# Optimization experiments

Hardware: AMD Instinct MI355X
Metric: run time of the kernel (lower is better)

## Reference

```python
import jax, jax.numpy as jnp
import numpy as np

INPUT_DIM = 128
HIDDEN_DIM = 64
BATCH = 256
SEQ_LEN = 1024


def _projectors(n):
    n_half = n // 2
    S = jnp.zeros((n, n), jnp.float32)
    S = S.at[:n_half, n_half:].set(jnp.eye(n_half))
    S = S.at[n_half:, :n_half].set(jnp.eye(n_half))
    I = jnp.eye(n, dtype=jnp.float32)
    return (I + S) / 2.0, (I - S) / 2.0


def setup_inputs() -> dict:
    key = jax.random.key(0)
    ks = jax.random.split(key, 7)
    x = jax.random.normal(ks[0], (BATCH, SEQ_LEN, INPUT_DIM), jnp.float32)
    A_plus = jax.random.normal(ks[1], (HIDDEN_DIM, HIDDEN_DIM), jnp.float32) * 0.1
    A_minus = jax.random.normal(ks[2], (HIDDEN_DIM, HIDDEN_DIM), jnp.float32) * 0.1
    # nn.Linear default init: U(-1/sqrt(fan_in), 1/sqrt(fan_in))
    b_in = 1.0 / np.sqrt(INPUT_DIM)
    W_in_w = jax.random.uniform(ks[3], (HIDDEN_DIM, INPUT_DIM), jnp.float32, -b_in, b_in)
    W_in_b = jax.random.uniform(ks[4], (HIDDEN_DIM,), jnp.float32, -b_in, b_in)
    b_out = 1.0 / np.sqrt(HIDDEN_DIM)
    W_out_w = jax.random.uniform(ks[5], (INPUT_DIM, HIDDEN_DIM), jnp.float32, -b_out, b_out)
    W_out_b = jax.random.uniform(ks[6], (INPUT_DIM,), jnp.float32, -b_out, b_out)
    bias = jnp.zeros((HIDDEN_DIM,), jnp.float32)
    return {"x": x, "A_plus": A_plus, "A_minus": A_minus,
            "W_in_w": W_in_w, "W_in_b": W_in_b,
            "W_out_w": W_out_w, "W_out_b": W_out_b, "bias": bias}


def reference(x, A_plus, A_minus, W_in_w, W_in_b, W_out_w, W_out_b, bias):
    B, T, _ = x.shape
    H = bias.shape[0]
    P_plus, P_minus = _projectors(H)
    # W_comm = P+ A+ P+ + P- A- P-
    W_comm = P_plus @ A_plus @ P_plus + P_minus @ A_minus @ P_minus
    # Precompute input projection for all timesteps (one big GEMM): (B,T,H)
    inp = jnp.einsum('bti,hi->bth', x, W_in_w) + W_in_b + bias
    inp_t = jnp.transpose(inp, (1, 0, 2))  # (T,B,H)

    def step(h, u_t):
        h = jnp.tanh(h @ W_comm.T + u_t)
        return h, None

    h0 = jnp.zeros((B, H), x.dtype)
    hidden, _ = jax.lax.scan(step, h0, inp_t)
    predictions = hidden @ W_out_w.T + W_out_b  # (B, input_dim)
    return predictions, hidden
```

## Files before the change

kernel.cpp:

```cpp
#include <hip/hip_runtime.h>
#include <hip/hip_bf16.h>

#define BB 256
#define TT 1024
#define II 128
#define HH 64

#define PRESCALE 2.8853900817779268f

typedef float    f32x4_t __attribute__((ext_vector_type(4)));
typedef _Float16 h16x2   __attribute__((ext_vector_type(2)));
typedef _Float16 h16x4   __attribute__((ext_vector_type(4)));
typedef _Float16 h16x8   __attribute__((ext_vector_type(8)));
typedef __fp16   p16x2   __attribute__((ext_vector_type(2)));

union UH2 { unsigned u; h16x2 h; p16x2 p; };
union U4H8 { uint4 u; h16x8 h; };
union B128 { uint4 u; h16x2 h[4]; };

__device__ __forceinline__ float tanh_pre(float a){
  float e = __builtin_amdgcn_exp2f(a);
  return __builtin_fmaf(-2.0f, __builtin_amdgcn_rcpf(1.0f + e), 1.0f);
}

#if __has_builtin(__builtin_amdgcn_fdot2)
__device__ __forceinline__ float fdot2f(h16x2 a, h16x2 b, float c){
  return __builtin_amdgcn_fdot2(a, b, c, false);
}
#else
__device__ __forceinline__ float fdot2f(h16x2 a, h16x2 b, float c){
  return __builtin_fmaf((float)a[1], (float)b[1], __builtin_fmaf((float)a[0], (float)b[0], c));
}
#endif

__global__ void k_prep(const float* __restrict__ Ap, const float* __restrict__ Am,
                       const float* __restrict__ Winw,
                       const float* __restrict__ Winb, const float* __restrict__ bias,
                       float* __restrict__ wsf, unsigned* __restrict__ whf,
                       unsigned short* __restrict__ wsb){
  const int tid = threadIdx.x;
  for (int e = tid; e < 4096; e += 256){
    int i = e >> 6, j = e & 63;
    int is = i ^ 32, js = j ^ 32;
    float wp = Ap[i*64+j] + Ap[i*64+js] + Ap[is*64+j] + Ap[is*64+js];
    float wm = Am[i*64+j] - Am[i*64+js] - Am[is*64+j] + Am[is*64+js];
    wsf[e] = 0.25f * (wp + wm) * PRESCALE;
  }
  if (tid < 64) wsf[4096 + tid] = (Winb[tid] + bias[tid]) * PRESCALE;
  for (int e = tid; e < 8192; e += 256){
    int j = e & 7, lane = (e >> 3) & 63, fidx = e >> 9;
    int ks = fidx >> 2, nt = fidx & 3, l15 = lane & 15, q = lane >> 4;
    union { _Float16 f; unsigned short s; } cv;
    cv.f = (_Float16)(Winw[(nt*16 + l15)*II + ks*32 + q*8 + j] * PRESCALE);
    wsb[e] = cv.s;
  }
  __syncthreads();
  for (int e = tid; e < 2048; e += 256){
    int i = e >> 5, jp = e & 31;
    UH2 p;
    p.h[0] = (_Float16)wsf[i*64 + 2*jp];
    p.h[1] = (_Float16)wsf[i*64 + 2*jp + 1];
    whf[e] = p.u;
  }
}

__global__ __launch_bounds__(256, 1) void k_fused(const float* __restrict__ x,
                                                  const float* __restrict__ wsf,
                                                  const unsigned* __restrict__ whf,
                                                  const unsigned short* __restrict__ wsb,
                                                  const float* __restrict__ Wout,
                                                  const float* __restrict__ Woutb,
                                                  float* __restrict__ out){
  extern __shared__ unsigned char smem[];
  unsigned short* Us    = (unsigned short*)smem;
  unsigned*       flags = (unsigned*)(smem + 131072);
  unsigned*       Hb    = (unsigned*)(smem + 131072 + 256);

  const int b    = blockIdx.x;
  const int tid  = threadIdx.x;
  const int lane = tid & 63;
  const int wave = tid >> 6;
  const int l15  = lane & 15;
  const int q    = lane >> 4;

  if (tid < 64) flags[tid] = 0u;
  __syncthreads();

  if (wave != 0){
    h16x8 bfr[4][4];
    #pragma unroll
    for (int ks = 0; ks < 4; ++ks)
      #pragma unroll
      for (int nt = 0; nt < 4; ++nt)
        bfr[ks][nt] = *(const h16x8*)(wsb + ((ks*4 + nt)*64 + lane)*8);

    float bcv[4];
    #pragma unroll
    for (int nt = 0; nt < 4; ++nt) bcv[nt] = wsf[4096 + nt*16 + l15];

    const float* xb = x + (long)b * (TT * II);

    #pragma unroll 1
    for (int tile = wave - 1; tile < 64; tile += 3){
      const int trow = tile * 16;
      const float* xa = xb + (trow + l15) * II + q*8;
      h16x8 afr[4];
      #pragma unroll
      for (int ks = 0; ks < 4; ++ks){
        float4 a0 = *(const float4*)(xa + ks*32);
        float4 a1 = *(const float4*)(xa + ks*32 + 4);
        U4H8 v;
        UH2 p0, p1, p2, p3;
        p0.p = __builtin_amdgcn_cvt_pkrtz(a0.x, a0.y);
        p1.p = __builtin_amdgcn_cvt_pkrtz(a0.z, a0.w);
        p2.p = __builtin_amdgcn_cvt_pkrtz(a1.x, a1.y);
        p3.p = __builtin_amdgcn_cvt_pkrtz(a1.z, a1.w);
        v.u.x = p0.u; v.u.y = p1.u; v.u.z = p2.u; v.u.w = p3.u;
        afr[ks] = v.h;
      }
      f32x4_t acc[4];
      #pragma unroll
      for (int nt = 0; nt < 4; ++nt){
        acc[nt][0]=bcv[nt]; acc[nt][1]=bcv[nt]; acc[nt][2]=bcv[nt]; acc[nt][3]=bcv[nt];
      }
      #pragma unroll
      for (int ks = 0; ks < 4; ++ks){
        #pragma unroll
        for (int nt = 0; nt < 4; ++nt){
          acc[nt] = __builtin_amdgcn_mfma_f32_16x16x32_f16(afr[ks], bfr[ks][nt], acc[nt], 0, 0, 0);
        }
      }
      const int tg = tile*4 + q;
      #pragma unroll
      for (int nt = 0; nt < 4; ++nt){
        UH2 lo, hi;
        lo.p = __builtin_amdgcn_cvt_pkrtz(acc[nt][0], acc[nt][1]);
        hi.p = __builtin_amdgcn_cvt_pkrtz(acc[nt][2], acc[nt][3]);
        uint2 pk; pk.x = lo.u; pk.y = hi.u;
        *(uint2*)&Us[(tg*64 + nt*16 + l15) * 4] = pk;
      }
      __threadfence_block();
      if (lane == 0)
        __hip_atomic_store(&flags[tile], 1u, __ATOMIC_RELEASE, __HIP_MEMORY_SCOPE_WORKGROUP);
    }
    return;
  }

  h16x2 w[32];
  {
    const uint4* wr = (const uint4*)(whf + lane * 32);
    #pragma unroll
    for (int j4 = 0; j4 < 8; ++j4){
      uint4 v = wr[j4];
      UH2 c0, c1, c2, c3;
      c0.u = v.x; c1.u = v.y; c2.u = v.z; c3.u = v.w;
      w[4*j4+0] = c0.h; w[4*j4+1] = c1.h; w[4*j4+2] = c2.h; w[4*j4+3] = c3.h;
    }
  }

  while (!__hip_atomic_load(&flags[0], __ATOMIC_ACQUIRE, __HIP_MEMORY_SCOPE_WORKGROUP)) {}

  const h16x4* Ul = (const h16x4*)Us;
  h16x4 uc = Ul[0*64 + lane];
  h16x4 u1 = Ul[1*64 + lane];

  const bool wlane = !(lane & 1);

  float h = 0.0f;
  int last_ready = 0;
  #pragma unroll 1
  for (int tile = 0; tile < 64; ++tile){
    int wt = tile + 1; if (wt > 63) wt = 63;
    if (wt > last_ready){
      while (!__hip_atomic_load(&flags[wt], __ATOMIC_ACQUIRE, __HIP_MEMORY_SCOPE_WORKGROUP)) {}
      last_ready = wt;
    }
    #pragma unroll
    for (int tgl = 0; tgl < 4; ++tgl){
      const int tg = tile*4 + tgl;
      int tp = tg + 2; if (tp > TT/4 - 1) tp = TT/4 - 1;
      h16x4 u2 = Ul[tp*64 + lane];
      float ug0 = (float)uc[0], ug1 = (float)uc[1], ug2 = (float)uc[2], ug3 = (float)uc[3];
      #pragma unroll
      for (int g = 0; g < 4; ++g){
        float ugv = (g==0) ? ug0 : (g==1) ? ug1 : (g==2) ? ug2 : ug3;
        unsigned nbu = (unsigned)__builtin_amdgcn_mov_dpp(__float_as_uint(h), 0xB1, 0xF, 0xF, true);
        UH2 hp; hp.p = __builtin_amdgcn_cvt_pkrtz(h, __uint_as_float(nbu));
        if (wlane) Hb[lane >> 1] = hp.u;
        __asm__ volatile("" ::: "memory");
        __builtin_amdgcn_sched_barrier(0);
        B128 hv[8];
        const uint4* Hr = (const uint4*)Hb;
        #pragma unroll
        for (int r = 0; r < 8; ++r) hv[r].u = Hr[r];
        float a0 = ugv, a1 = 0.0f, a2 = 0.0f, a3 = 0.0f;
        #pragma unroll
        for (int jp = 0; jp < 32; jp += 4){
          a0 = fdot2f(w[jp+0], hv[(jp+0)>>2].h[(jp+0)&3], a0);
          a1 = fdot2f(w[jp+1], hv[(jp+1)>>2].h[(jp+1)&3], a1);
          a2 = fdot2f(w[jp+2], hv[(jp+2)>>2].h[(jp+2)&3], a2);
          a3 = fdot2f(w[jp+3], hv[(jp+3)>>2].h[(jp+3)&3], a3);
        }
        h = tanh_pre((a0 + a1) + (a2 + a3));
      }
      uc = u1; u1 = u2;
    }
  }

  unsigned hu = __float_as_uint(h);
  float p0 = Woutb[lane];
  float p1 = Woutb[lane + 64];
  #pragma unroll 8
  for (int j = 0; j < 64; ++j){
    float hj = __uint_as_float(__builtin_amdgcn_readlane(hu, j));
    p0 = __builtin_fmaf(Wout[lane * HH + j],        hj, p0);
    p1 = __builtin_fmaf(Wout[(lane + 64) * HH + j], hj, p1);
  }
  out[b * 128 + lane]           = p0;
  out[b * 128 + 64 + lane]      = p1;
  out[BB * 128 + b * 64 + lane] = h;
}

extern "C" void kernel_launch(void* const* d_in, const int* in_sizes, int n_in,
                              void* d_out, int out_size, void* d_ws, size_t ws_size,
                              hipStream_t stream){
  const float* x     = (const float*)d_in[0];
  const float* Ap    = (const float*)d_in[1];
  const float* Am    = (const float*)d_in[2];
  const float* Winw  = (const float*)d_in[3];
  const float* Winb  = (const float*)d_in[4];
  const float* Woutw = (const float*)d_in[5];
  const float* Woutb = (const float*)d_in[6];
  const float* bias  = (const float*)d_in[7];

  float*          wsf = (float*)d_ws;
  unsigned*       whf = (unsigned*)((char*)d_ws + 16640);
  unsigned short* wsb = (unsigned short*)((char*)d_ws + 24832);

  float* out = (float*)d_out;

  hipFuncSetAttribute((const void*)k_fused,
                      hipFuncAttributeMaxDynamicSharedMemorySize, 131456);

  hipLaunchKernelGGL(k_prep,  dim3(1),   dim3(256), 0,      stream, Ap, Am, Winw, Winb, bias, wsf, whf, wsb);
  hipLaunchKernelGGL(k_fused, dim3(BB),  dim3(256), 131456, stream, x, wsf, whf, wsb, Woutw, Woutb, out);
}
```

Before: 339.5 us.

## Block-diagonalize recurrent matrix via symmetric/antisymmetric projector basis

Uses the projector structure of W_comm to split the 64x64 recurrence into two independent 32x32 blocks acting on the sum and difference of hidden halves. Each lane forms h±h_swap with a permlane32 swap, writes the packed values to a per-half LDS slot, and does 16 fdot2 instead of 32. A second swap recombines the outputs into the original basis. This halves the per-step dot-product work and LDS reads on the serial critical path, at the cost of two cross-half swaps per step and extra fp16 rounding of the combined values.

Measured after the change: 311.4 us. 8.3% less time.

```diff
diff --git a/kernel.cpp b/kernel.cpp
--- a/kernel.cpp
+++ b/kernel.cpp
@@ -30,6 +30,18 @@
 #else
 __device__ __forceinline__ float fdot2f(h16x2 a, h16x2 b, float c){
   return __builtin_fmaf((float)a[1], (float)b[1], __builtin_fmaf((float)a[0], (float)b[0], c));
+}
+#endif
+
+#if __has_builtin(__builtin_amdgcn_permlane32_swap)
+__device__ __forceinline__ float half_swap(float v){
+  unsigned vu = __float_as_uint(v);
+  auto r = __builtin_amdgcn_permlane32_swap(vu, vu, false, false);
+  return __uint_as_float(((unsigned)r[0]) ^ ((unsigned)r[1]) ^ vu);
+}
+#else
+__device__ __forceinline__ float half_swap(float v){
+  return __shfl_xor(v, 32, 64);
 }
 #endif
 
@@ -39,28 +51,28 @@
                        float* __restrict__ wsf, unsigned* __restrict__ whf,
                        unsigned short* __restrict__ wsb){
   const int tid = threadIdx.x;
-  for (int e = tid; e < 4096; e += 256){
-    int i = e >> 6, j = e & 63;
-    int is = i ^ 32, js = j ^ 32;
-    float wp = Ap[i*64+j] + Ap[i*64+js] + Ap[is*64+j] + Ap[is*64+js];
-    float wm = Am[i*64+j] - Am[i*64+js] - Am[is*64+j] + Am[is*64+js];
-    wsf[e] = 0.25f * (wp + wm) * PRESCALE;
-  }
   if (tid < 64) wsf[4096 + tid] = (Winb[tid] + bias[tid]) * PRESCALE;
+  for (int e = tid; e < 1024; e += 256){
+    int lane = e >> 4, jp = e & 15, row = lane & 31, j = 2*jp;
+    float v0, v1;
+    if (lane < 32){
+      v0 = 0.25f*PRESCALE*(Ap[row*64+j]     + Ap[row*64+j+32]     + Ap[(row+32)*64+j]     + Ap[(row+32)*64+j+32]);
+      v1 = 0.25f*PRESCALE*(Ap[row*64+j+1]   + Ap[row*64+j+33]     + Ap[(row+32)*64+j+1]   + Ap[(row+32)*64+j+33]);
+    } else {
+      v0 = 0.25f*PRESCALE*(Am[row*64+j]     - Am[row*64+j+32]     - Am[(row+32)*64+j]     + Am[(row+32)*64+j+32]);
+      v1 = 0.25f*PRESCALE*(Am[row*64+j+1]   - Am[row*64+j+33]     - Am[(row+32)*64+j+1]   + Am[(row+32)*64+j+33]);
+    }
+    UH2 p;
+    p.h[0] = (_Float16)v0;
+    p.h[1] = (_Float16)v1;
+    whf[e] = p.u;
+  }
   for (int e = tid; e < 8192; e += 256){
     int j = e & 7, lane = (e >> 3) & 63, fidx = e >> 9;
     int ks = fidx >> 2, nt = fidx & 3, l15 = lane & 15, q = lane >> 4;
     union { _Float16 f; unsigned short s; } cv;
     cv.f = (_Float16)(Winw[(nt*16 + l15)*II + ks*32 + q*8 + j] * PRESCALE);
     wsb[e] = cv.s;
-  }
-  __syncthreads();
-  for (int e = tid; e < 2048; e += 256){
-    int i = e >> 5, jp = e & 31;
-    UH2 p;
-    p.h[0] = (_Float16)wsf[i*64 + 2*jp];
-    p.h[1] = (_Float16)wsf[i*64 + 2*jp + 1];
-    whf[e] = p.u;
   }
 }
 
@@ -146,11 +158,11 @@
     return;
   }
 
-  h16x2 w[32];
+  h16x2 w[16];
   {
-    const uint4* wr = (const uint4*)(whf + lane * 32);
-    #pragma unroll
-    for (int j4 = 0; j4 < 8; ++j4){
+    const uint4* wr = (const uint4*)(whf + lane * 16);
+    #pragma unroll
+    for (int j4 = 0; j4 < 4; ++j4){
       uint4 v = wr[j4];
       UH2 c0, c1, c2, c3;
       c0.u = v.x; c1.u = v.y; c2.u = v.z; c3.u = v.w;
@@ -158,13 +170,16 @@
     }
   }
 
+  const bool  lo    = (lane < 32);
+  const float sgn   = lo ? 1.0f : -1.0f;
+  const int   hslot = (lane >> 1) + (lane & 1) * 32;
+  const uint4* Hr   = (const uint4*)((const unsigned char*)Hb + (lane & 32) * 2);
+
   while (!__hip_atomic_load(&flags[0], __ATOMIC_ACQUIRE, __HIP_MEMORY_SCOPE_WORKGROUP)) {}
 
   const h16x4* Ul = (const h16x4*)Us;
   h16x4 uc = Ul[0*64 + lane];
   h16x4 u1 = Ul[1*64 + lane];
-
-  const bool wlane = !(lane & 1);
 
   float h = 0.0f;
   int last_ready = 0;
@@ -184,24 +199,28 @@
       #pragma unroll
       for (int g = 0; g < 4; ++g){
         float ugv = (g==0) ? ug0 : (g==1) ? ug1 : (g==2) ? ug2 : ug3;
-        unsigned nbu = (unsigned)__builtin_amdgcn_mov_dpp(__float_as_uint(h), 0xB1, 0xF, 0xF, true);
-        UH2 hp; hp.p = __builtin_amdgcn_cvt_pkrtz(h, __uint_as_float(nbu));
-        if (wlane) Hb[lane >> 1] = hp.u;
+        float hsw = half_swap(h);
+        float sd  = __builtin_fmaf(h, sgn, hsw);
+        unsigned nbu = (unsigned)__builtin_amdgcn_mov_dpp(__float_as_uint(sd), 0xB1, 0xF, 0xF, true);
+        UH2 hp; hp.p = __builtin_amdgcn_cvt_pkrtz(sd, __uint_as_float(nbu));
+        Hb[hslot] = hp.u;
         __asm__ volatile("" ::: "memory");
         __builtin_amdgcn_sched_barrier(0);
-        B128 hv[8];
-        const uint4* Hr = (const uint4*)Hb;
+        B128 hv[4];
         #pragma unroll
-        for (int r = 0; r < 8; ++r) hv[r].u = Hr[r];
-        float a0 = ugv, a1 = 0.0f, a2 = 0.0f, a3 = 0.0f;
+        for (int r = 0; r < 4; ++r) hv[r].u = Hr[r];
+        float a0 = 0.0f, a1 = 0.0f, a2 = 0.0f, a3 = 0.0f;
         #pragma unroll
-        for (int jp = 0; jp < 32; jp += 4){
+        for (int jp = 0; jp < 16; jp += 4){
           a0 = fdot2f(w[jp+0], hv[(jp+0)>>2].h[(jp+0)&3], a0);
           a1 = fdot2f(w[jp+1], hv[(jp+1)>>2].h[(jp+1)&3], a1);
           a2 = fdot2f(w[jp+2], hv[(jp+2)>>2].h[(jp+2)&3], a2);
           a3 = fdot2f(w[jp+3], hv[(jp+3)>>2].h[(jp+3)&3], a3);
         }
-        h = tanh_pre((a0 + a1) + (a2 + a3));
+        float z = (a0 + a1) + (a2 + a3);
+        float zsw = half_swap(z);
+        float a = __builtin_fmaf(z, sgn, zsw) + ugv;
+        h = tanh_pre(a);
       }
       uc = u1; u1 = u2;
     }
@@ -240,8 +259,8 @@
   float* out = (float*)d_out;
 
   hipFuncSetAttribute((const void*)k_fused,
-                      hipFuncAttributeMaxDynamicSharedMemorySize, 131456);
+                      hipFuncAttributeMaxDynamicSharedMemorySize, 131584);
 
   hipLaunchKernelGGL(k_prep,  dim3(1),   dim3(256), 0,      stream, Ap, Am, Winw, Winb, bias, wsf, whf, wsb);
-  hipLaunchKernelGGL(k_fused, dim3(BB),  dim3(256), 131456, stream, x, wsf, whf, wsb, Woutw, Woutb, out);
-}
+  hipLaunchKernelGGL(k_fused, dim3(BB),  dim3(256), 131584, stream, x, wsf, whf, wsb, Woutw, Woutb, out);
+}
```
